# Kernel optimization log

Measured on AMD Instinct MI355X. Metric: run time of the kernel, lower is better.

The kernel has to match this reference:

```python
import jax, jax.numpy as jnp
import numpy as np

W = 4  # kernel_size

def setup_inputs() -> dict:
    key = jax.random.key(0)
    k1, k2, k3, k4 = jax.random.split(key, 4)
    B, T, D, H = 4, 4096, 2048, 256
    x = jax.random.normal(k1, (B, T, D), dtype=jnp.float32)
    # stored as [in, out] (transpose of torch Linear convention)
    w1 = jax.random.normal(k2, (D, H), dtype=jnp.float32) * 0.02
    w2 = jax.random.normal(k3, (H, D * W), dtype=jnp.float32) * 0.02
    b2 = jax.random.normal(k4, (D * W,), dtype=jnp.float32) * 0.02
    return {"x": x, "w1": w1, "w2": w2, "b2": b2}

def reference(x, w1, w2, b2):
    # x: [B, T, D]
    B, T, D = x.shape
    # kernel generator: Linear -> silu -> Linear(+bias)
    h = jax.nn.silu(jnp.einsum('btd,dh->bth', x, w1))
    flat = jnp.einsum('bth,ho->bto', h, w2) + b2          # [B, T, D*W]
    kernels = flat.reshape(B, T, D, W)                    # per-token depthwise kernels
    # causal depthwise dynamic conv: out[t] = sum_w k[t, :, w] * x[t - (W-1) + w]
    xp = jnp.pad(x, ((0, 0), (W - 1, 0), (0, 0)))         # left-pad time by W-1
    out = jnp.zeros_like(x)
    for w in range(W):  # W is a small static constant (4)
        out = out + kernels[..., w] * xp[:, w:w + T, :]
    return jax.nn.silu(out)
```

## Files before the change

kernel.cpp:

```cpp
#include <hip/hip_runtime.h>

typedef unsigned short u16;
typedef unsigned int   u32;
typedef __attribute__((ext_vector_type(8))) short short8;
typedef __attribute__((ext_vector_type(4))) float floatx4;

#define T_DIM 4096
#define D_DIM 2048
#define H_DIM 256
#define M_DIM 16384
#define NFLAT 8192

__device__ __forceinline__ u16 f2bf(float f) {
  union { float f; u32 u; } c; c.f = f;
  u32 x = c.u;
  x += 0x7FFFu + ((x >> 16) & 1u);
  return (u16)(x >> 16);
}
__device__ __forceinline__ u32 pk2(float a, float b) {
  return (u32)f2bf(a) | ((u32)f2bf(b) << 16);
}

__device__ __forceinline__ void glds16(const void* g, void* l) {
  __builtin_amdgcn_global_load_lds(
      (const __attribute__((address_space(1))) void*)g,
      (__attribute__((address_space(3))) void*)l, 16, 0, 0);
}

__global__ void __launch_bounds__(256) tr_cvt_all(const float* __restrict__ w1,
                                                  u16* __restrict__ w1t,
                                                  const float* __restrict__ w2,
                                                  u16* __restrict__ w2t) {
  __shared__ u16 tile[32][33];
  int bid = blockIdx.x;
  const float* src; u16* dst; int R, C, c0, r0;
  if (bid < 512) {
    src = w1; dst = w1t; R = D_DIM; C = H_DIM;
    c0 = (bid & 7) * 32; r0 = (bid >> 3) * 32;
  } else {
    int b = bid - 512;
    src = w2; dst = w2t; R = H_DIM; C = NFLAT;
    c0 = (b & 255) * 32; r0 = (b >> 8) * 32;
  }
  const int tx = threadIdx.x & 31;
  const int ty = threadIdx.x >> 5;
  #pragma unroll
  for (int i = ty; i < 32; i += 8)
    tile[i][tx] = f2bf(src[(size_t)(r0 + i) * C + (c0 + tx)]);
  __syncthreads();
  #pragma unroll
  for (int i = ty; i < 32; i += 8)
    dst[(size_t)(c0 + i) * R + (r0 + tx)] = tile[tx][i];
}

__global__ void __launch_bounds__(256) gemm1_silu(const float* __restrict__ X,
                                                  const u16* __restrict__ Bt,
                                                  u16* __restrict__ H) {
  __shared__ __align__(16) u16 As[2][32][64];
  __shared__ __align__(16) u16 Bs[2][256][64];
  const int tid  = threadIdx.x;
  const int lane = tid & 63, l15 = lane & 15, quad = lane >> 4;
  const int wv   = tid >> 6;
  const int m0   = blockIdx.x * 32;
  const int srow = lane >> 3, sc = lane & 7;

  floatx4 acc[2][4];
  const floatx4 zf = {0.f, 0.f, 0.f, 0.f};
  #pragma unroll
  for (int i = 0; i < 2; ++i)
    #pragma unroll
    for (int j = 0; j < 4; ++j) acc[i][j] = zf;

  float4 fA0[2], fA1[2];

#define G1_LOADA(KT, FW)                                                      \
  {                                                                           \
    int row = tid >> 3, g = tid & 7;                                          \
    const float* xs = &X[(size_t)(m0 + row) * D_DIM + (KT) * 64 + g * 8];     \
    FW[0] = *(const float4*)xs;                                               \
    FW[1] = *(const float4*)(xs + 4);                                         \
  }

#define G1_WRITEA(BUF, FW)                                                    \
  {                                                                           \
    int row = tid >> 3, g = tid & 7, c = g ^ (row & 7);                       \
    uint4 pk;                                                                 \
    pk.x = pk2(FW[0].x, FW[0].y);                                             \
    pk.y = pk2(FW[0].z, FW[0].w);                                             \
    pk.z = pk2(FW[1].x, FW[1].y);                                             \
    pk.w = pk2(FW[1].z, FW[1].w);                                             \
    *(uint4*)&As[BUF][row][c * 8] = pk;                                       \
  }

#define G1_STAGEB(KT, BUF)                                                    \
  _Pragma("unroll")                                                           \
  for (int ci = 0; ci < 8; ++ci) {                 \
    int ch  = wv * 8 + ci;                                                    \
    int row = ch * 8 + srow;                             \
    glds16(&Bt[(size_t)row * D_DIM + (KT) * 64 + (sc ^ (row & 7)) * 8],       \
           (char*)Bs + (BUF) * 32768 + ch * 1024);                            \
  }

#define G1_STAGE_NEXT(T, BUFN, FW)                                            \
  if ((T) + 1 < 32) {                                                         \
    G1_WRITEA(BUFN, FW);                                                      \
    __builtin_amdgcn_sched_barrier(0);                                        \
    G1_STAGEB((T) + 1, BUFN);                                                 \
    __builtin_amdgcn_sched_barrier(0);                                        \
    if ((T) + 3 < 32) { G1_LOADA((T) + 3, FW); }                              \
  }

#define G1_COMPUTE(BUFC)                                                      \
  {                                                                           \
    short8 af[2][2], bfr[4][2];                                               \
    _Pragma("unroll")                                                         \
    for (int ks = 0; ks < 2; ++ks) {                                          \
      _Pragma("unroll")                                                       \
      for (int mi = 0; mi < 2; ++mi) {                                        \
        int row = mi * 16 + l15;                                              \
        af[mi][ks] = *(const short8*)&As[BUFC][row][((ks * 4 + quad) ^ (row & 7)) * 8]; \
      }                                                                       \
      _Pragma("unroll")                                                       \
      for (int ni = 0; ni < 4; ++ni) {                                        \
        int row = wv * 64 + ni * 16 + l15;                                    \
        bfr[ni][ks] = *(const short8*)&Bs[BUFC][row][((ks * 4 + quad) ^ (row & 7)) * 8]; \
      }                                                                       \
    }                                                                         \
    _Pragma("unroll")                                                         \
    for (int ks = 0; ks < 2; ++ks)                                            \
      _Pragma("unroll")                                                       \
      for (int mi = 0; mi < 2; ++mi)                                          \
        _Pragma("unroll")                                                     \
        for (int ni = 0; ni < 4; ++ni)                                        \
          acc[mi][ni] = __builtin_amdgcn_mfma_f32_16x16x32_bf16(af[mi][ks], bfr[ni][ks], acc[mi][ni], 0, 0, 0); \
  }

#define G1_SYNC(T)                                                            \
  if ((T) + 1 < 32) {                                                         \
    if ((T) <= 28) { asm volatile("s_waitcnt vmcnt(2)" ::: "memory"); }       \
    else           { asm volatile("s_waitcnt vmcnt(0)" ::: "memory"); }       \
    asm volatile("s_waitcnt lgkmcnt(0)" ::: "memory");                        \
    __builtin_amdgcn_sched_barrier(0);                                        \
    __builtin_amdgcn_s_barrier();                                             \
    __builtin_amdgcn_sched_barrier(0);                                        \
  }

  G1_LOADA(0, fA0);
  G1_LOADA(1, fA1);
  G1_WRITEA(0, fA0);
  __builtin_amdgcn_sched_barrier(0);
  G1_STAGEB(0, 0);
  __builtin_amdgcn_sched_barrier(0);
  G1_LOADA(2, fA0);
  asm volatile("s_waitcnt vmcnt(2)" ::: "memory");
  asm volatile("s_waitcnt lgkmcnt(0)" ::: "memory");
  __builtin_amdgcn_sched_barrier(0);
  __builtin_amdgcn_s_barrier();
  __builtin_amdgcn_sched_barrier(0);

  for (int tt = 0; tt < 32; tt += 2) {
    G1_STAGE_NEXT(tt, 1, fA1);
    G1_COMPUTE(0);
    G1_SYNC(tt);
    G1_STAGE_NEXT(tt + 1, 0, fA0);
    G1_COMPUTE(1);
    G1_SYNC(tt + 1);
  }

  #pragma unroll
  for (int mi = 0; mi < 2; ++mi)
    #pragma unroll
    for (int ni = 0; ni < 4; ++ni)
      #pragma unroll
      for (int r = 0; r < 4; ++r) {
        float v = acc[mi][ni][r];
        v = v / (1.f + __expf(-v));
        int row = m0 + mi * 16 + quad * 4 + r;
        int col = wv * 64 + ni * 16 + l15;
        H[(size_t)row * H_DIM + col] = f2bf(v);
      }
#undef G1_LOADA
#undef G1_WRITEA
#undef G1_STAGEB
#undef G1_STAGE_NEXT
#undef G1_COMPUTE
#undef G1_SYNC
}

__global__ void __launch_bounds__(256) gemm2_conv_silu(const u16* __restrict__ Hin,
                                                       const u16* __restrict__ Bt,
                                                       const float* __restrict__ bias,
                                                       const float* __restrict__ X,
                                                       float* __restrict__ Out) {
  __shared__ __align__(16) u16 As[128][64];
  __shared__ __align__(16) u16 Bs[128][64];
  const int tid  = threadIdx.x;
  const int lane = tid & 63, l15 = lane & 15, quad = lane >> 4;
  const int wv   = tid >> 6, wy = wv >> 1, wx = wv & 1;
  const int m0   = blockIdx.y * 128;
  const int d0   = blockIdx.x * 32;
  const int srow = lane >> 3, sc = lane & 7;

  floatx4 acc[4][4];
  const floatx4 zf = {0.f, 0.f, 0.f, 0.f};
  #pragma unroll
  for (int i = 0; i < 4; ++i)
    #pragma unroll
    for (int j = 0; j < 4; ++j) acc[i][j] = zf;

  for (int k0 = 0; k0 < H_DIM; k0 += 64) {
    __syncthreads();
    #pragma unroll
    for (int ci = 0; ci < 4; ++ci) {
      int ch  = ci * 4 + wv;
      int row = ch * 8 + srow;
      int g   = (sc ^ (row & 7)) * 8;
      glds16(&Hin[(size_t)(m0 + row) * H_DIM + k0 + g], (char*)As + ch * 1024);
      int fc = (d0 + ((row >> 6) << 4) + (row & 15)) * 4 + ((row >> 4) & 3);
      glds16(&Bt[(size_t)fc * H_DIM + k0 + g], (char*)Bs + ch * 1024);
    }
    __syncthreads();
    short8 af[4][2], bfr[4][2];
    #pragma unroll
    for (int ks = 0; ks < 2; ++ks) {
      #pragma unroll
      for (int mi = 0; mi < 4; ++mi) {
        int row = wy * 64 + mi * 16 + l15;
        af[mi][ks] = *(const short8*)&As[row][((ks * 4 + quad) ^ (row & 7)) * 8];
      }
      #pragma unroll
      for (int ni = 0; ni < 4; ++ni) {
        int row = wx * 64 + ni * 16 + l15;
        bfr[ni][ks] = *(const short8*)&Bs[row][((ks * 4 + quad) ^ (row & 7)) * 8];
      }
    }
    #pragma unroll
    for (int ks = 0; ks < 2; ++ks)
      #pragma unroll
      for (int mi = 0; mi < 4; ++mi)
        #pragma unroll
        for (int ni = 0; ni < 4; ++ni)
          acc[mi][ni] = __builtin_amdgcn_mfma_f32_16x16x32_bf16(af[mi][ks], bfr[ni][ks], acc[mi][ni], 0, 0, 0);
  }

  const int d     = d0 + wx * 16 + l15;
  const float4 bv = *(const float4*)&bias[(size_t)d * 4];
  const int tbase = m0 & (T_DIM - 1);
  const int bbase = m0 - tbase;
  const float* xcol = &X[(size_t)bbase * D_DIM + d];
  float* ocol       = &Out[(size_t)m0 * D_DIM + d];

  #pragma unroll
  for (int mi = 0; mi < 4; ++mi) {
    int t0 = wy * 64 + mi * 16 + quad * 4;
    int tq = tbase + t0;
    float xv[7];
    #pragma unroll
    for (int j = 0; j < 7; ++j) {
      int tt = tq - 3 + j;
      xv[j] = (tt >= 0) ? xcol[(size_t)tt * D_DIM] : 0.f;
    }
    #pragma unroll
    for (int r = 0; r < 4; ++r) {
      float c0 = acc[mi][0][r] + bv.x;
      float c1 = acc[mi][1][r] + bv.y;
      float c2 = acc[mi][2][r] + bv.z;
      float c3 = acc[mi][3][r] + bv.w;
      float o  = c0 * xv[r] + c1 * xv[r + 1] + c2 * xv[r + 2] + c3 * xv[r + 3];
      float y  = o / (1.f + __expf(-o));
      ocol[(size_t)(t0 + r) * D_DIM] = y;
    }
  }
}

extern "C" void kernel_launch(void* const* d_in, const int* in_sizes, int n_in,
                              void* d_out, int out_size, void* d_ws, size_t ws_size,
                              hipStream_t stream) {
  const float* x  = (const float*)d_in[0];
  const float* w1 = (const float*)d_in[1];
  const float* w2 = (const float*)d_in[2];
  const float* b2 = (const float*)d_in[3];
  float* out = (float*)d_out;

  u16* w1t = (u16*)d_ws;
  u16* w2t = w1t + (size_t)H_DIM * D_DIM;
  u16* h   = w2t + (size_t)NFLAT * H_DIM;

  tr_cvt_all<<<512 + 2048, 256, 0, stream>>>(w1, w1t, w2, w2t);
  gemm1_silu<<<M_DIM / 32, 256, 0, stream>>>(x, w1t, h);
  gemm2_conv_silu<<<dim3(D_DIM / 32, M_DIM / 128), 256, 0, stream>>>(h, w2t, b2, x, out);
}
```

Measured before the change: 330.2 us.

## Triple-buffer gemm2 LDS staging with async prefetch two k-tiles ahead

```diff
diff --git a/kernel.cpp b/kernel.cpp
--- a/kernel.cpp
+++ b/kernel.cpp
@@ -192,14 +192,14 @@
                                                        const float* __restrict__ bias,
                                                        const float* __restrict__ X,
                                                        float* __restrict__ Out) {
-  __shared__ __align__(16) u16 As[128][64];
-  __shared__ __align__(16) u16 Bs[128][64];
+  __shared__ __align__(16) u16 As[3][128][32];
+  __shared__ __align__(16) u16 Bs[3][128][32];
   const int tid  = threadIdx.x;
   const int lane = tid & 63, l15 = lane & 15, quad = lane >> 4;
   const int wv   = tid >> 6, wy = wv >> 1, wx = wv & 1;
   const int m0   = blockIdx.y * 128;
   const int d0   = blockIdx.x * 32;
-  const int srow = lane >> 3, sc = lane & 7;
+  const int rloc = lane >> 2, hh = lane & 3;
 
   floatx4 acc[4][4];
   const floatx4 zf = {0.f, 0.f, 0.f, 0.f};
@@ -208,40 +208,69 @@
     #pragma unroll
     for (int j = 0; j < 4; ++j) acc[i][j] = zf;
 
-  for (int k0 = 0; k0 < H_DIM; k0 += 64) {
-    __syncthreads();
-    #pragma unroll
-    for (int ci = 0; ci < 4; ++ci) {
-      int ch  = ci * 4 + wv;
-      int row = ch * 8 + srow;
-      int g   = (sc ^ (row & 7)) * 8;
-      glds16(&Hin[(size_t)(m0 + row) * H_DIM + k0 + g], (char*)As + ch * 1024);
-      int fc = (d0 + ((row >> 6) << 4) + (row & 15)) * 4 + ((row >> 4) & 3);
-      glds16(&Bt[(size_t)fc * H_DIM + k0 + g], (char*)Bs + ch * 1024);
+#define G2_STAGE(KT, BUF)                                                     \
+  _Pragma("unroll")                                                           \
+  for (int ci = 0; ci < 2; ++ci) {                                            \
+    int ch  = wv * 2 + ci;                                                    \
+    int row = ch * 16 + rloc;                                     \
+    int g   = hh ^ ((row >> 1) & 3);                 \
+    glds16(&Hin[(size_t)(m0 + row) * H_DIM + (KT) * 32 + g * 8],              \
+           (char*)As + (BUF) * 8192 + ch * 1024);                             \
+    int fc  = (d0 + ((row >> 6) << 4) + (row & 15)) * 4 + ((row >> 4) & 3);   \
+    glds16(&Bt[(size_t)fc * H_DIM + (KT) * 32 + g * 8],                       \
+           (char*)Bs + (BUF) * 8192 + ch * 1024);                             \
+  }
+
+#define G2_COMPUTE(BUF)                                                       \
+  {                                                                           \
+    short8 af[4], bfr[4];                                                     \
+    _Pragma("unroll")                                                         \
+    for (int mi = 0; mi < 4; ++mi) {                                          \
+      int row = wy * 64 + mi * 16 + l15;                                      \
+      int h   = quad ^ ((row >> 1) & 3);                                      \
+      af[mi] = *(const short8*)((const char*)As + (BUF) * 8192 + row * 64 + h * 16); \
+    }                                                                         \
+    _Pragma("unroll")                                                         \
+    for (int ni = 0; ni < 4; ++ni) {                                          \
+      int row = wx * 64 + ni * 16 + l15;                                      \
+      int h   = quad ^ ((row >> 1) & 3);                                      \
+      bfr[ni] = *(const short8*)((const char*)Bs + (BUF) * 8192 + row * 64 + h * 16); \
+    }                                                                         \
+    _Pragma("unroll")                                                         \
+    for (int mi = 0; mi < 4; ++mi)                                            \
+      _Pragma("unroll")                                                       \
+      for (int ni = 0; ni < 4; ++ni)                                          \
+        acc[mi][ni] = __builtin_amdgcn_mfma_f32_16x16x32_bf16(af[mi], bfr[ni], acc[mi][ni], 0, 0, 0); \
+  }
+
+#define G2_SYNC(NWAIT)                                                        \
+  asm volatile("s_waitcnt vmcnt(" #NWAIT ")" ::: "memory");                   \
+  asm volatile("s_waitcnt lgkmcnt(0)" ::: "memory");                          \
+  __builtin_amdgcn_sched_barrier(0);                                          \
+  __builtin_amdgcn_s_barrier();                                               \
+  __builtin_amdgcn_sched_barrier(0);
+
+  G2_STAGE(0, 0);
+  __builtin_amdgcn_sched_barrier(0);
+  G2_STAGE(1, 1);
+  __builtin_amdgcn_sched_barrier(0);
+  G2_SYNC(4)
+
+  #pragma unroll
+  for (int t = 0; t < 8; ++t) {
+    if (t + 2 < 8) {
+      G2_STAGE(t + 2, (t + 2) % 3);
+      __builtin_amdgcn_sched_barrier(0);
     }
-    __syncthreads();
-    short8 af[4][2], bfr[4][2];
-    #pragma unroll
-    for (int ks = 0; ks < 2; ++ks) {
-      #pragma unroll
-      for (int mi = 0; mi < 4; ++mi) {
-        int row = wy * 64 + mi * 16 + l15;
-        af[mi][ks] = *(const short8*)&As[row][((ks * 4 + quad) ^ (row & 7)) * 8];
-      }
-      #pragma unroll
-      for (int ni = 0; ni < 4; ++ni) {
-        int row = wx * 64 + ni * 16 + l15;
-        bfr[ni][ks] = *(const short8*)&Bs[row][((ks * 4 + quad) ^ (row & 7)) * 8];
-      }
+    G2_COMPUTE(t % 3);
+    if (t + 1 < 8) {
+      if (t + 2 < 8) { G2_SYNC(4) }
+      else           { G2_SYNC(0) }
     }
-    #pragma unroll
-    for (int ks = 0; ks < 2; ++ks)
-      #pragma unroll
-      for (int mi = 0; mi < 4; ++mi)
-        #pragma unroll
-        for (int ni = 0; ni < 4; ++ni)
-          acc[mi][ni] = __builtin_amdgcn_mfma_f32_16x16x32_bf16(af[mi][ks], bfr[ni][ks], acc[mi][ni], 0, 0, 0);
-  }
+  }
+#undef G2_STAGE
+#undef G2_COMPUTE
+#undef G2_SYNC
 
   const int d     = d0 + wx * 16 + l15;
   const float4 bv = *(const float4*)&bias[(size_t)d * 4];
```

After: 343.5 us. +4.0%, slower.
